# Performance work log

Measured on AMD Instinct MI355X. Metric: run time of the kernel, lower is better.

Reference implementation:

```python
import jax, jax.numpy as jnp
import numpy as np

N, E, G = 400000, 2500000, 512
IN_F, H, C = 7, 32, 2
EPS = 1e-5


def setup_inputs() -> dict:
    key = jax.random.key(0)
    ks = jax.random.split(key, 12)
    x = jax.random.normal(ks[0], (N, IN_F), jnp.float32)
    edge_index = jax.random.randint(ks[1], (2, E), 0, N, dtype=jnp.int64)
    edge_attr = jax.random.uniform(ks[2], (E,), jnp.float32)
    batch = jnp.sort(jax.random.randint(ks[3], (N,), 0, G, dtype=jnp.int64))

    def lin(k, i, o):
        return (jax.random.normal(k, (i, o), jnp.float32) / np.sqrt(i)).astype(jnp.float32)

    params = dict(
        W0=lin(ks[4], IN_F, H), b0=jnp.zeros((H,), jnp.float32),
        W1=lin(ks[5], H, H),    b1=jnp.zeros((H,), jnp.float32),
        W2=lin(ks[6], H, H),    b2=jnp.zeros((H,), jnp.float32),
        W3=lin(ks[7], H, H),    b3=jnp.zeros((H,), jnp.float32),
        bn_g=jnp.ones((3, H), jnp.float32), bn_b=jnp.zeros((3, H), jnp.float32),
        Wm0=lin(ks[8], H, H),   bm0=jnp.zeros((H,), jnp.float32),
        bnm_g=jnp.ones((H,), jnp.float32), bnm_b=jnp.zeros((H,), jnp.float32),
        Wm1=lin(ks[9], H, C),   bm1=jnp.zeros((C,), jnp.float32),
    )
    return {"x": x, "edge_index": edge_index, "edge_attr": edge_attr, "batch": batch, **params}


def _batchnorm(h, g, b):
    # training-mode batch norm over the node/graph axis
    m = h.mean(axis=0)
    v = h.var(axis=0)
    return (h - m) * jax.lax.rsqrt(v + EPS) * g + b


def _gcn_forward(x, edge_index, edge_attr, batch,
                 W0, b0, W1, b1, W2, b2, W3, b3, bn_g, bn_b,
                 Wm0, bm0, bnm_g, bnm_b, Wm1, bm1):
    row, col = edge_index[0], edge_index[1]
    # add self-loops with weight 1 (GCNConv default), then symmetric normalization
    loop = jnp.arange(N, dtype=row.dtype)
    row = jnp.concatenate([row, loop])
    col = jnp.concatenate([col, loop])
    w = jnp.concatenate([edge_attr, jnp.ones((N,), edge_attr.dtype)])
    deg = jax.ops.segment_sum(w, col, num_segments=N)
    dinv = jnp.where(deg > 0, jax.lax.rsqrt(jnp.maximum(deg, EPS)), 0.0)
    norm = dinv[row] * w * dinv[col]  # [E+N]

    def conv(h, W, b):
        h = h @ W                                    # [N,H] dense transform
        msg = norm[:, None] * h[row]                 # gather + scale
        return jax.ops.segment_sum(msg, col, num_segments=N) + b  # scatter-add

    h = jax.nn.relu(_batchnorm(conv(x, W0, b0), bn_g[0], bn_b[0]))
    h = jax.nn.relu(_batchnorm(conv(h, W1, b1), bn_g[1], bn_b[1]))
    h = jax.nn.relu(_batchnorm(conv(h, W2, b2), bn_g[2], bn_b[2]))
    h = conv(h, W3, b3)                              # last GCN layer: no norm/act

    g = jax.ops.segment_sum(h, batch, num_segments=G)  # global_add_pool -> [G,H]
    g = jax.nn.relu(_batchnorm(g @ Wm0 + bm0, bnm_g, bnm_b))
    return g @ Wm1 + bm1                             # [G,C]


def reference(x, edge_index, edge_attr, batch,
              W0, b0, W1, b1, W2, b2, W3, b3, bn_g, bn_b,
              Wm0, bm0, bnm_g, bnm_b, Wm1, bm1):
    return _gcn_forward(x, edge_index, edge_attr, batch,
                        W0, b0, W1, b1, W2, b2, W3, b3, bn_g, bn_b,
                        Wm0, bm0, bnm_g, bnm_b, Wm1, bm1)
```

## Files before the change

kernel.cpp:

```cpp
#include <hip/hip_runtime.h>

#define TPB 256
#define RBITS 10
#define RSZ   1024
#define BMAX  512
#define CHUNK 4096
constexpr float EPSV = 1e-5f;

__device__ __forceinline__ float bf2f(unsigned short u) {
  return __uint_as_float((unsigned)u << 16);
}
__device__ __forceinline__ unsigned short f2bf(float f) {
  unsigned u = __float_as_uint(f);
  return (unsigned short)((u + 0x7fffu + ((u >> 16) & 1u)) >> 16);
}


__global__ void k_bcnt(const int* __restrict__ col, int* __restrict__ bcnt, int E, int B) {
  __shared__ int h[BMAX];
  const int tid = threadIdx.x;
  for (int i = tid; i < B; i += TPB) h[i] = 0;
  __syncthreads();
  const int e0 = blockIdx.x * CHUNK;
  for (int k = tid; k < CHUNK; k += TPB) {
    int i = e0 + k;
    if (i < E) atomicAdd(&h[col[i] >> RBITS], 1);
  }
  __syncthreads();
  for (int i = tid; i < B; i += TPB)
    if (h[i]) atomicAdd(&bcnt[i], h[i]);
}

__global__ void k_bscan(const int* __restrict__ bcnt, int* __restrict__ bbase,
                        int* __restrict__ bcur, int B, int E) {
  __shared__ int red[BMAX];
  const int tid = threadIdx.x;
  int v = (tid < B) ? bcnt[tid] : 0;
  red[tid] = v;
  __syncthreads();
  for (int off = 1; off < BMAX; off <<= 1) {
    int u = (tid >= off) ? red[tid - off] : 0;
    __syncthreads();
    red[tid] += u;
    __syncthreads();
  }
  int excl = red[tid] - v;
  if (tid < B) { bbase[tid] = excl; bcur[tid] = excl; }
  if (tid == 0) bbase[B] = E;
}

__global__ void k_binfill(const int* __restrict__ row, const int* __restrict__ col,
                          const float* __restrict__ w, int* __restrict__ bcur,
                          uint2* __restrict__ buck, int E, int B) {
  __shared__ int h[BMAX], base[BMAX], cur[BMAX];
  const int tid = threadIdx.x;
  for (int i = tid; i < B; i += TPB) { h[i] = 0; cur[i] = 0; }
  __syncthreads();
  const int e0 = blockIdx.x * CHUNK;
  for (int k = tid; k < CHUNK; k += TPB) {
    int i = e0 + k;
    if (i < E) atomicAdd(&h[col[i] >> RBITS], 1);
  }
  __syncthreads();
  for (int i = tid; i < B; i += TPB)
    base[i] = h[i] ? atomicAdd(&bcur[i], h[i]) : 0;
  __syncthreads();
  for (int k = tid; k < CHUNK; k += TPB) {
    int i = e0 + k;
    if (i >= E) continue;
    int c = col[i];
    int b = c >> RBITS;
    int pos = base[b] + atomicAdd(&cur[b], 1);
    unsigned lc = (unsigned)(c & (RSZ - 1));
    buck[pos] = make_uint2((unsigned)row[i] | (lc << 19), __float_as_uint(w[i]));
  }
}

__global__ __launch_bounds__(256) void k_bucket(const uint2* __restrict__ buck,
                                                const int* __restrict__ bbase,
                                                int* __restrict__ ptr, float* __restrict__ dinv,
                                                uint2* __restrict__ pk, int N, int E) {
  __shared__ int cnt[RSZ];
  __shared__ float wsum[RSZ];
  __shared__ int lofs[RSZ];
  __shared__ int red[256];
  const int bk = blockIdx.x, tid = threadIdx.x;
  const int n0 = bk << RBITS;
  const int nloc = min(RSZ, N - n0);
  for (int i = tid; i < RSZ; i += 256) { cnt[i] = 0; wsum[i] = 0.f; }
  __syncthreads();
  const int e0 = bbase[bk], e1 = bbase[bk + 1];
  for (int i = e0 + tid; i < e1; i += 256) {
    uint2 e = buck[i];
    int lc = e.x >> 19;
    atomicAdd(&cnt[lc], 1);
    atomicAdd(&wsum[lc], __uint_as_float(e.y));
  }
  __syncthreads();
  int a = cnt[tid * 4], b = cnt[tid * 4 + 1], c = cnt[tid * 4 + 2], d = cnt[tid * 4 + 3];
  int l1 = a, l2 = a + b, l3 = a + b + c, s = a + b + c + d;
  red[tid] = s;
  __syncthreads();
  for (int off = 1; off < 256; off <<= 1) {
    int u = (tid >= off) ? red[tid - off] : 0;
    __syncthreads();
    red[tid] += u;
    __syncthreads();
  }
  int tb = red[tid] - s;
  lofs[tid * 4] = tb; lofs[tid * 4 + 1] = tb + l1;
  lofs[tid * 4 + 2] = tb + l2; lofs[tid * 4 + 3] = tb + l3;
  __syncthreads();
  for (int i = tid; i < nloc; i += 256) {
    ptr[n0 + i] = e0 + lofs[i];
    dinv[n0 + i] = rsqrtf(1.0f + wsum[i]);
  }
  for (int i = tid; i < RSZ; i += 256) cnt[i] = 0;
  __syncthreads();
  for (int i = e0 + tid; i < e1; i += 256) {
    uint2 e = buck[i];
    int lc = e.x >> 19;
    int pos = e0 + lofs[lc] + atomicAdd(&cnt[lc], 1);
    float wdc = __uint_as_float(e.y) * rsqrtf(1.0f + wsum[lc]);
    pk[pos] = make_uint2(e.x & 524287u, __float_as_uint(wdc));
  }
  if (bk == 0 && tid == 0) ptr[N] = E;
}

__global__ void k_nrme(uint2* __restrict__ pk, const float* __restrict__ dinv, int E) {
  int e = blockIdx.x * blockDim.x + threadIdx.x;
  if (e < E) {
    uint2 v = pk[e];
    pk[e].y = __float_as_uint(__uint_as_float(v.y) * dinv[v.x]);
  }
}


__global__ void k_transform0(const float* __restrict__ in, const float* __restrict__ W,
                             unsigned short* __restrict__ t, int N) {
  __shared__ float Ws[7 * 32];
  __shared__ float hs[8 * 7];
  const int tid = threadIdx.x;
  const int n0 = blockIdx.x * 8;
  if (tid < 7 * 32) Ws[tid] = W[tid];
  if (tid < 8 * 7) {
    int node = n0 + tid / 7;
    hs[tid] = (node < N) ? in[n0 * 7 + tid] : 0.0f;
  }
  __syncthreads();
  const int j = tid >> 5, c = tid & 31;
  const int node = n0 + j;
  if (node < N) {
    float acc = 0.0f;
#pragma unroll
    for (int k = 0; k < 7; ++k) acc += hs[j * 7 + k] * Ws[k * 32 + c];
    t[(size_t)node * 32 + c] = f2bf(acc);
  }
}

__global__ __launch_bounds__(256) void k_transform(
    const uint4* __restrict__ in4, const float* __restrict__ W,
    const float* __restrict__ gstats, const float* __restrict__ gamma,
    const float* __restrict__ beta, float invN, uint2* __restrict__ t2, int N) {
  __shared__ float Ws[1024];
  __shared__ float hs[32 * 33];
  __shared__ float ssb[64];
  const int tid = threadIdx.x;
  const int n0 = blockIdx.x * 32;
#pragma unroll
  for (int k = 0; k < 4; ++k) Ws[k * 256 + tid] = W[k * 256 + tid];
  if (tid < 32) {
    float m = gstats[tid] * invN;
    float v = gstats[32 + tid] * invN - m * m;
    float sc = gamma[tid] * rsqrtf(v + EPSV);
    ssb[tid] = sc;
    ssb[32 + tid] = beta[tid] - m * sc;
  }
  __syncthreads();
  if (tid < 128) {
    const int r = tid >> 2, q = tid & 3;
    const int node = n0 + r;
    uint4 v = make_uint4(0, 0, 0, 0);
    if (node < N) v = in4[(size_t)node * 4 + q];
    float* h = &hs[r * 33 + q * 8];
    const float* sc = &ssb[q * 8];
    const float* sh = &ssb[32 + q * 8];
    h[0] = fmaxf(__uint_as_float(v.x << 16) * sc[0] + sh[0], 0.f);
    h[1] = fmaxf(__uint_as_float(v.x & 0xffff0000u) * sc[1] + sh[1], 0.f);
    h[2] = fmaxf(__uint_as_float(v.y << 16) * sc[2] + sh[2], 0.f);
    h[3] = fmaxf(__uint_as_float(v.y & 0xffff0000u) * sc[3] + sh[3], 0.f);
    h[4] = fmaxf(__uint_as_float(v.z << 16) * sc[4] + sh[4], 0.f);
    h[5] = fmaxf(__uint_as_float(v.z & 0xffff0000u) * sc[5] + sh[5], 0.f);
    h[6] = fmaxf(__uint_as_float(v.w << 16) * sc[6] + sh[6], 0.f);
    h[7] = fmaxf(__uint_as_float(v.w & 0xffff0000u) * sc[7] + sh[7], 0.f);
  }
  __syncthreads();
  const int j = tid >> 3;
  const int c0 = (tid & 7) * 4;
  const int node = n0 + j;
  if (node < N) {
    float a0 = 0.f, a1 = 0.f, a2 = 0.f, a3 = 0.f;
#pragma unroll
    for (int k = 0; k < 32; ++k) {
      float v = hs[j * 33 + k];
      const float* w = &Ws[k * 32 + c0];
      a0 += v * w[0]; a1 += v * w[1]; a2 += v * w[2]; a3 += v * w[3];
    }
    uint2 o;
    o.x = (unsigned)f2bf(a0) | ((unsigned)f2bf(a1) << 16);
    o.y = (unsigned)f2bf(a2) | ((unsigned)f2bf(a3) << 16);
    t2[(size_t)node * 8 + (tid & 7)] = o;
  }
}


__device__ __forceinline__ void fma8(float* acc, uint4 v, float wt) {
  acc[0] += wt * __uint_as_float(v.x << 16);
  acc[1] += wt * __uint_as_float(v.x & 0xffff0000u);
  acc[2] += wt * __uint_as_float(v.y << 16);
  acc[3] += wt * __uint_as_float(v.y & 0xffff0000u);
  acc[4] += wt * __uint_as_float(v.z << 16);
  acc[5] += wt * __uint_as_float(v.z & 0xffff0000u);
  acc[6] += wt * __uint_as_float(v.w << 16);
  acc[7] += wt * __uint_as_float(v.w & 0xffff0000u);
}

__global__ __launch_bounds__(256, 4) void k_gather(
    const uint2* __restrict__ pk, const int* __restrict__ ptr,
    const float* __restrict__ dinv, const uint4* __restrict__ t4,
    uint4* __restrict__ out4, int N) {
  const int n = blockIdx.x * 256 + threadIdx.x;
  if (n >= N) return;
  const int p0 = ptr[n], p1 = ptr[n + 1];
  const float dvn = dinv[n];
  float acc[32];
  {
    const float wt = dvn * dvn;
    const size_t rb = (size_t)n * 4;
    uint4 A = t4[rb], B = t4[rb + 1], C = t4[rb + 2], D = t4[rb + 3];
#pragma unroll
    for (int k = 0; k < 32; ++k) acc[k] = 0.f;
    fma8(acc, A, wt); fma8(acc + 8, B, wt); fma8(acc + 16, C, wt); fma8(acc + 24, D, wt);
  }
  for (int p = p0; p < p1; ++p) {
    uint2 e = pk[p];
    const float wt = __uint_as_float(e.y);
    const size_t rb = (size_t)e.x * 4;
    uint4 A = t4[rb], B = t4[rb + 1], C = t4[rb + 2], D = t4[rb + 3];
    fma8(acc, A, wt); fma8(acc + 8, B, wt); fma8(acc + 16, C, wt); fma8(acc + 24, D, wt);
  }
  const size_t ob = (size_t)n * 4;
#pragma unroll
  for (int q = 0; q < 4; ++q) {
    uint4 o;
    o.x = (unsigned)f2bf(acc[q * 8 + 0]) | ((unsigned)f2bf(acc[q * 8 + 1]) << 16);
    o.y = (unsigned)f2bf(acc[q * 8 + 2]) | ((unsigned)f2bf(acc[q * 8 + 3]) << 16);
    o.z = (unsigned)f2bf(acc[q * 8 + 4]) | ((unsigned)f2bf(acc[q * 8 + 5]) << 16);
    o.w = (unsigned)f2bf(acc[q * 8 + 6]) | ((unsigned)f2bf(acc[q * 8 + 7]) << 16);
    out4[ob + q] = o;
  }
}


__global__ void k_stats(const uint4* __restrict__ x4, float* __restrict__ gstats, int nquads) {
  __shared__ float ls[64];
  const int tid = threadIdx.x;
  if (tid < 64) ls[tid] = 0.f;
  __syncthreads();
  const int q = tid & 3;
  float s[8], sq[8];
#pragma unroll
  for (int k = 0; k < 8; ++k) { s[k] = 0.f; sq[k] = 0.f; }
  for (int idx = blockIdx.x * TPB + tid; idx < nquads; idx += gridDim.x * TPB) {
    uint4 v = x4[idx];
    float f0 = __uint_as_float(v.x << 16), f1 = __uint_as_float(v.x & 0xffff0000u);
    float f2 = __uint_as_float(v.y << 16), f3 = __uint_as_float(v.y & 0xffff0000u);
    float f4 = __uint_as_float(v.z << 16), f5 = __uint_as_float(v.z & 0xffff0000u);
    float f6 = __uint_as_float(v.w << 16), f7 = __uint_as_float(v.w & 0xffff0000u);
    s[0] += f0; sq[0] += f0 * f0;  s[1] += f1; sq[1] += f1 * f1;
    s[2] += f2; sq[2] += f2 * f2;  s[3] += f3; sq[3] += f3 * f3;
    s[4] += f4; sq[4] += f4 * f4;  s[5] += f5; sq[5] += f5 * f5;
    s[6] += f6; sq[6] += f6 * f6;  s[7] += f7; sq[7] += f7 * f7;
  }
#pragma unroll
  for (int k = 0; k < 8; ++k) {
    int c = q * 8 + k;
    atomicAdd(&ls[c], s[k]);
    atomicAdd(&ls[32 + c], sq[k]);
  }
  __syncthreads();
  if (tid < 64) unsafeAtomicAdd(&gstats[tid], ls[tid]);
}


__global__ __launch_bounds__(256) void k_pool(
    const uint4* __restrict__ h4, const int* __restrict__ batch,
    const float* __restrict__ b3, float* __restrict__ pool, int N) {
  __shared__ float red[64 * 33];
  const int g = blockIdx.x, tid = threadIdx.x;
  int lo = 0, hi = N;
  while (lo < hi) { int mid = (lo + hi) >> 1; if (batch[mid] < g) lo = mid + 1; else hi = mid; }
  const int start = lo;
  hi = N;
  while (lo < hi) { int mid = (lo + hi) >> 1; if (batch[mid] < g + 1) lo = mid + 1; else hi = mid; }
  const int end = lo;
  const int j = tid >> 2, q = tid & 3;
  float a[8];
#pragma unroll
  for (int k = 0; k < 8; ++k) a[k] = 0.f;
  for (int i = start + j; i < end; i += 64) {
    uint4 v = h4[(size_t)i * 4 + q];
    a[0] += __uint_as_float(v.x << 16); a[1] += __uint_as_float(v.x & 0xffff0000u);
    a[2] += __uint_as_float(v.y << 16); a[3] += __uint_as_float(v.y & 0xffff0000u);
    a[4] += __uint_as_float(v.z << 16); a[5] += __uint_as_float(v.z & 0xffff0000u);
    a[6] += __uint_as_float(v.w << 16); a[7] += __uint_as_float(v.w & 0xffff0000u);
  }
#pragma unroll
  for (int k = 0; k < 8; ++k) red[j * 33 + q * 8 + k] = a[k];
  __syncthreads();
  for (int off = 32; off >= 1; off >>= 1) {
    if (j < off) {
#pragma unroll
      for (int k = 0; k < 8; ++k)
        red[j * 33 + q * 8 + k] += red[(j + off) * 33 + q * 8 + k];
    }
    __syncthreads();
  }
  if (tid < 32) pool[g * 32 + tid] = red[tid] + (float)(end - start) * b3[tid];
}


__global__ void k_mlpz(const float* __restrict__ pool, const float* __restrict__ Wm0,
                       const float* __restrict__ bm0, float* __restrict__ z,
                       float* __restrict__ mstats) {
  __shared__ float Ws[32 * 32];
  __shared__ float ps[8 * 32];
  __shared__ float ls[TPB], lq[TPB];
  const int tid = threadIdx.x;
  const int g0 = blockIdx.x * 8;
  for (int k = tid; k < 1024; k += TPB) Ws[k] = Wm0[k];
  if (tid < 256) ps[tid] = pool[g0 * 32 + tid];
  __syncthreads();
  const int j = tid >> 5, c = tid & 31;
  float acc = bm0[c];
#pragma unroll
  for (int k = 0; k < 32; ++k) acc += ps[j * 32 + k] * Ws[k * 32 + c];
  z[(g0 + j) * 32 + c] = acc;
  ls[tid] = acc;
  lq[tid] = acc * acc;
  __syncthreads();
  for (int off = 128; off >= 32; off >>= 1) {
    if (tid < off) { ls[tid] += ls[tid + off]; lq[tid] += lq[tid + off]; }
    __syncthreads();
  }
  if (tid < 32) {
    unsafeAtomicAdd(&mstats[tid], ls[tid]);
    unsafeAtomicAdd(&mstats[32 + tid], lq[tid]);
  }
}

__global__ void k_mlpfin(const float* __restrict__ z, const float* __restrict__ mstats,
                         const float* __restrict__ bng, const float* __restrict__ bnb,
                         const float* __restrict__ Wm1, const float* __restrict__ bm1,
                         float* __restrict__ out) {
  __shared__ float sc[32], sh[32], w1[64];
  const int tid = threadIdx.x;
  if (tid < 32) {
    float m = mstats[tid] * (1.0f / 512.0f);
    float v = mstats[32 + tid] * (1.0f / 512.0f) - m * m;
    float s = bng[tid] * rsqrtf(v + EPSV);
    sc[tid] = s;
    sh[tid] = bnb[tid] - m * s;
  }
  if (tid < 64) w1[tid] = Wm1[tid];
  __syncthreads();
  const int g = tid >> 1, o = tid & 1;
  float acc = bm1[o];
#pragma unroll
  for (int c = 0; c < 32; ++c) {
    float hc = fmaxf(z[g * 32 + c] * sc[c] + sh[c], 0.f);
    acc += hc * w1[c * 2 + o];
  }
  out[tid] = acc;
}


extern "C" void kernel_launch(void* const* d_in, const int* in_sizes, int n_in,
                              void* d_out, int out_size, void* d_ws, size_t ws_size,
                              hipStream_t stream) {
  const float* x     = (const float*)d_in[0];
  const int*   ei    = (const int*)d_in[1];
  const float* ea    = (const float*)d_in[2];
  const int*   batch = (const int*)d_in[3];
  const float* W0    = (const float*)d_in[4];
  const float* W1    = (const float*)d_in[6];
  const float* W2    = (const float*)d_in[8];
  const float* W3    = (const float*)d_in[10];
  const float* b3    = (const float*)d_in[11];
  const float* bng   = (const float*)d_in[12];
  const float* bnb   = (const float*)d_in[13];
  const float* Wm0   = (const float*)d_in[14];
  const float* bm0   = (const float*)d_in[15];
  const float* bnmg  = (const float*)d_in[16];
  const float* bnmb  = (const float*)d_in[17];
  const float* Wm1   = (const float*)d_in[18];
  const float* bm1   = (const float*)d_in[19];
  float* out = (float*)d_out;

  const int N = in_sizes[3];
  const int E = in_sizes[2];
  const int* row = ei;
  const int* col = ei + E;
  const int B = (N + RSZ - 1) >> RBITS;

  char* wsb = (char*)d_ws;
  auto alloc = [&](size_t bytes) { char* p = wsb; wsb += (bytes + 255) & ~size_t(255); return p; };
  int*   bcnt  = (int*)alloc((size_t)(BMAX + 1) * 4);
  int*   bbase = (int*)alloc((size_t)(BMAX + 1) * 4);
  int*   bcur  = (int*)alloc((size_t)BMAX * 4);
  int*   ptr   = (int*)alloc((size_t)(N + 1) * 4);
  uint2* buck  = (uint2*)alloc((size_t)E * 8);
  uint2* pk    = (uint2*)alloc((size_t)E * 8);
  float* dinv  = (float*)alloc((size_t)N * 4);
  unsigned short* B0 = (unsigned short*)alloc((size_t)N * 32 * 2);
  unsigned short* B1 = (unsigned short*)alloc((size_t)N * 32 * 2);
  float* stats = (float*)alloc(4 * 64 * 4);
  float* pool  = (float*)alloc(512 * 32 * 4);
  float* zbuf  = (float*)alloc(512 * 32 * 4);

  hipMemsetAsync(bcnt, 0, (size_t)(BMAX + 1) * 4, stream);
  hipMemsetAsync(stats, 0, 4 * 64 * 4, stream);

  const int nb_c = (E + CHUNK - 1) / CHUNK;
  const int nb_e = (E + 255) / 256;
  const int nb_t0 = (N + 7) / 8;
  const int nb_t = (N + 31) / 32;
  const int nb_g = (N + 255) / 256;
  const int nquads = N * 4;
  const float invN = 1.0f / (float)N;
  float* mstats = stats + 192;

  k_bcnt<<<nb_c, TPB, 0, stream>>>(col, bcnt, E, B);
  k_bscan<<<1, BMAX, 0, stream>>>(bcnt, bbase, bcur, B, E);
  k_binfill<<<nb_c, TPB, 0, stream>>>(row, col, ea, bcur, buck, E, B);
  k_bucket<<<B, 256, 0, stream>>>(buck, bbase, ptr, dinv, pk, N, E);
  k_nrme<<<nb_e, 256, 0, stream>>>(pk, dinv, E);

  k_transform0<<<nb_t0, TPB, 0, stream>>>(x, W0, B0, N);
  k_gather<<<nb_g, 256, 0, stream>>>(pk, ptr, dinv, (const uint4*)B0, (uint4*)B1, N);
  k_stats<<<1024, TPB, 0, stream>>>((const uint4*)B1, stats, nquads);

  k_transform<<<nb_t, 256, 0, stream>>>((const uint4*)B1, W1, stats, bng, bnb, invN,
                                        (uint2*)B0, N);
  k_gather<<<nb_g, 256, 0, stream>>>(pk, ptr, dinv, (const uint4*)B0, (uint4*)B1, N);
  k_stats<<<1024, TPB, 0, stream>>>((const uint4*)B1, stats + 64, nquads);

  k_transform<<<nb_t, 256, 0, stream>>>((const uint4*)B1, W2, stats + 64, bng + 32, bnb + 32,
                                        invN, (uint2*)B0, N);
  k_gather<<<nb_g, 256, 0, stream>>>(pk, ptr, dinv, (const uint4*)B0, (uint4*)B1, N);
  k_stats<<<1024, TPB, 0, stream>>>((const uint4*)B1, stats + 128, nquads);

  k_transform<<<nb_t, 256, 0, stream>>>((const uint4*)B1, W3, stats + 128, bng + 64, bnb + 64,
                                        invN, (uint2*)B0, N);
  k_gather<<<nb_g, 256, 0, stream>>>(pk, ptr, dinv, (const uint4*)B0, (uint4*)B1, N);

  k_pool<<<512, 256, 0, stream>>>((const uint4*)B1, batch, b3, pool, N);
  k_mlpz<<<64, TPB, 0, stream>>>(pool, Wm0, bm0, zbuf, mstats);
  k_mlpfin<<<1, 1024, 0, stream>>>(zbuf, mstats, bnmg, bnmb, Wm1, bm1, out);
}
```

Baseline: 740.0 us.

## Aggregate raw 7-feature input before first transform and fuse layer-0 stats

Uses linearity (A·X)·W = A·(X·W) to gather the 7-wide input packed as 8 bf16 values (16 bytes per node) instead of the 32-wide transformed features (64 bytes per node). The matmul by W0 then runs after aggregation in a new kernel that also reduces the batch-norm sums, which removes one stats pass. The gather is templated on width and now prefetches the next edge record, so pk needs one padding entry. Converting x to bf16 before aggregation changes rounding slightly, and the prefetch reads one element past the valid edge range.

```diff
diff --git a/kernel.cpp b/kernel.cpp
--- a/kernel.cpp
+++ b/kernel.cpp
@@ -136,27 +136,74 @@
 }
 
 
-__global__ void k_transform0(const float* __restrict__ in, const float* __restrict__ W,
-                             unsigned short* __restrict__ t, int N) {
+__global__ void k_packx(const float* __restrict__ x, uint4* __restrict__ g, int N) {
+  int n = blockIdx.x * 256 + threadIdx.x;
+  if (n >= N) return;
+  const float* p = x + (size_t)n * 7;
+  unsigned b[8];
+#pragma unroll
+  for (int k = 0; k < 7; ++k) b[k] = f2bf(p[k]);
+  b[7] = 0;
+  uint4 o;
+  o.x = b[0] | (b[1] << 16); o.y = b[2] | (b[3] << 16);
+  o.z = b[4] | (b[5] << 16); o.w = b[6] | (b[7] << 16);
+  g[n] = o;
+}
+
+__global__ __launch_bounds__(256) void k_transform0b(
+    const uint4* __restrict__ g1, const float* __restrict__ W,
+    float* __restrict__ gstats, uint2* __restrict__ t2, int N) {
   __shared__ float Ws[7 * 32];
-  __shared__ float hs[8 * 7];
-  const int tid = threadIdx.x;
-  const int n0 = blockIdx.x * 8;
-  if (tid < 7 * 32) Ws[tid] = W[tid];
-  if (tid < 8 * 7) {
-    int node = n0 + tid / 7;
-    hs[tid] = (node < N) ? in[n0 * 7 + tid] : 0.0f;
-  }
-  __syncthreads();
-  const int j = tid >> 5, c = tid & 31;
+  __shared__ float hs[32 * 9];
+  __shared__ float sarr[64];
+  const int tid = threadIdx.x;
+  const int n0 = blockIdx.x * 32;
+  if (tid < 224) Ws[tid] = W[tid];
+  if (tid < 64) sarr[tid] = 0.f;
+  if (tid < 32) {
+    const int node = n0 + tid;
+    uint4 v = make_uint4(0, 0, 0, 0);
+    if (node < N) v = g1[node];
+    float* h = &hs[tid * 9];
+    h[0] = __uint_as_float(v.x << 16); h[1] = __uint_as_float(v.x & 0xffff0000u);
+    h[2] = __uint_as_float(v.y << 16); h[3] = __uint_as_float(v.y & 0xffff0000u);
+    h[4] = __uint_as_float(v.z << 16); h[5] = __uint_as_float(v.z & 0xffff0000u);
+    h[6] = __uint_as_float(v.w << 16); h[7] = 0.f;
+  }
+  __syncthreads();
+  const int j = tid >> 3, q = tid & 7, c0 = q * 4;
   const int node = n0 + j;
+  float a0 = 0.f, a1 = 0.f, a2 = 0.f, a3 = 0.f;
+#pragma unroll
+  for (int k = 0; k < 7; ++k) {
+    float v = hs[j * 9 + k];
+    const float* w = &Ws[k * 32 + c0];
+    a0 += v * w[0]; a1 += v * w[1]; a2 += v * w[2]; a3 += v * w[3];
+  }
   if (node < N) {
-    float acc = 0.0f;
-#pragma unroll
-    for (int k = 0; k < 7; ++k) acc += hs[j * 7 + k] * Ws[k * 32 + c];
-    t[(size_t)node * 32 + c] = f2bf(acc);
-  }
-}
+    uint2 o;
+    o.x = (unsigned)f2bf(a0) | ((unsigned)f2bf(a1) << 16);
+    o.y = (unsigned)f2bf(a2) | ((unsigned)f2bf(a3) << 16);
+    t2[(size_t)node * 8 + q] = o;
+  }
+  float q0 = a0 * a0, q1 = a1 * a1, q2 = a2 * a2, q3 = a3 * a3;
+#pragma unroll
+  for (int m = 8; m < 64; m <<= 1) {
+    a0 += __shfl_xor(a0, m, 64); a1 += __shfl_xor(a1, m, 64);
+    a2 += __shfl_xor(a2, m, 64); a3 += __shfl_xor(a3, m, 64);
+    q0 += __shfl_xor(q0, m, 64); q1 += __shfl_xor(q1, m, 64);
+    q2 += __shfl_xor(q2, m, 64); q3 += __shfl_xor(q3, m, 64);
+  }
+  if ((tid & 63) < 8) {
+    atomicAdd(&sarr[c0 + 0], a0); atomicAdd(&sarr[c0 + 1], a1);
+    atomicAdd(&sarr[c0 + 2], a2); atomicAdd(&sarr[c0 + 3], a3);
+    atomicAdd(&sarr[32 + c0 + 0], q0); atomicAdd(&sarr[32 + c0 + 1], q1);
+    atomicAdd(&sarr[32 + c0 + 2], q2); atomicAdd(&sarr[32 + c0 + 3], q3);
+  }
+  __syncthreads();
+  if (tid < 64) unsafeAtomicAdd(&gstats[tid], sarr[tid]);
+}
+
 
 __global__ __launch_bounds__(256) void k_transform(
     const uint4* __restrict__ in4, const float* __restrict__ W,
@@ -225,6 +272,7 @@
   acc[7] += wt * __uint_as_float(v.w & 0xffff0000u);
 }
 
+template <int Q>
 __global__ __launch_bounds__(256, 4) void k_gather(
     const uint2* __restrict__ pk, const int* __restrict__ ptr,
     const float* __restrict__ dinv, const uint4* __restrict__ t4,
@@ -233,31 +281,35 @@
   if (n >= N) return;
   const int p0 = ptr[n], p1 = ptr[n + 1];
   const float dvn = dinv[n];
-  float acc[32];
+  float acc[8 * Q];
+#pragma unroll
+  for (int k = 0; k < 8 * Q; ++k) acc[k] = 0.f;
   {
     const float wt = dvn * dvn;
-    const size_t rb = (size_t)n * 4;
-    uint4 A = t4[rb], B = t4[rb + 1], C = t4[rb + 2], D = t4[rb + 3];
-#pragma unroll
-    for (int k = 0; k < 32; ++k) acc[k] = 0.f;
-    fma8(acc, A, wt); fma8(acc + 8, B, wt); fma8(acc + 16, C, wt); fma8(acc + 24, D, wt);
-  }
-  for (int p = p0; p < p1; ++p) {
-    uint2 e = pk[p];
-    const float wt = __uint_as_float(e.y);
-    const size_t rb = (size_t)e.x * 4;
-    uint4 A = t4[rb], B = t4[rb + 1], C = t4[rb + 2], D = t4[rb + 3];
-    fma8(acc, A, wt); fma8(acc + 8, B, wt); fma8(acc + 16, C, wt); fma8(acc + 24, D, wt);
-  }
-  const size_t ob = (size_t)n * 4;
-#pragma unroll
-  for (int q = 0; q < 4; ++q) {
+    const size_t rb = (size_t)n * Q;
+#pragma unroll
+    for (int qq = 0; qq < Q; ++qq) fma8(acc + 8 * qq, t4[rb + qq], wt);
+  }
+  if (p0 < p1) {
+    uint2 e = pk[p0];
+    for (int p = p0; p < p1; ++p) {
+      uint2 en = pk[p + 1];
+      const float wt = __uint_as_float(e.y);
+      const size_t rb = (size_t)e.x * Q;
+#pragma unroll
+      for (int qq = 0; qq < Q; ++qq) fma8(acc + 8 * qq, t4[rb + qq], wt);
+      e = en;
+    }
+  }
+  const size_t ob = (size_t)n * Q;
+#pragma unroll
+  for (int qq = 0; qq < Q; ++qq) {
     uint4 o;
-    o.x = (unsigned)f2bf(acc[q * 8 + 0]) | ((unsigned)f2bf(acc[q * 8 + 1]) << 16);
-    o.y = (unsigned)f2bf(acc[q * 8 + 2]) | ((unsigned)f2bf(acc[q * 8 + 3]) << 16);
-    o.z = (unsigned)f2bf(acc[q * 8 + 4]) | ((unsigned)f2bf(acc[q * 8 + 5]) << 16);
-    o.w = (unsigned)f2bf(acc[q * 8 + 6]) | ((unsigned)f2bf(acc[q * 8 + 7]) << 16);
-    out4[ob + q] = o;
+    o.x = (unsigned)f2bf(acc[qq * 8 + 0]) | ((unsigned)f2bf(acc[qq * 8 + 1]) << 16);
+    o.y = (unsigned)f2bf(acc[qq * 8 + 2]) | ((unsigned)f2bf(acc[qq * 8 + 3]) << 16);
+    o.z = (unsigned)f2bf(acc[qq * 8 + 4]) | ((unsigned)f2bf(acc[qq * 8 + 5]) << 16);
+    o.w = (unsigned)f2bf(acc[qq * 8 + 6]) | ((unsigned)f2bf(acc[qq * 8 + 7]) << 16);
+    out4[ob + qq] = o;
   }
 }
 
@@ -420,8 +472,10 @@
   int*   bcur  = (int*)alloc((size_t)BMAX * 4);
   int*   ptr   = (int*)alloc((size_t)(N + 1) * 4);
   uint2* buck  = (uint2*)alloc((size_t)E * 8);
-  uint2* pk    = (uint2*)alloc((size_t)E * 8);
+  uint2* pk    = (uint2*)alloc((size_t)(E + 1) * 8);
   float* dinv  = (float*)alloc((size_t)N * 4);
+  uint4* G0    = (uint4*)alloc((size_t)N * 16);
+  uint4* G1    = (uint4*)alloc((size_t)N * 16);
   unsigned short* B0 = (unsigned short*)alloc((size_t)N * 32 * 2);
   unsigned short* B1 = (unsigned short*)alloc((size_t)N * 32 * 2);
   float* stats = (float*)alloc(4 * 64 * 4);
@@ -433,7 +487,6 @@
 
   const int nb_c = (E + CHUNK - 1) / CHUNK;
   const int nb_e = (E + 255) / 256;
-  const int nb_t0 = (N + 7) / 8;
   const int nb_t = (N + 31) / 32;
   const int nb_g = (N + 255) / 256;
   const int nquads = N * 4;
@@ -446,23 +499,23 @@
   k_bucket<<<B, 256, 0, stream>>>(buck, bbase, ptr, dinv, pk, N, E);
   k_nrme<<<nb_e, 256, 0, stream>>>(pk, dinv, E);
 
-  k_transform0<<<nb_t0, TPB, 0, stream>>>(x, W0, B0, N);
-  k_gather<<<nb_g, 256, 0, stream>>>(pk, ptr, dinv, (const uint4*)B0, (uint4*)B1, N);
-  k_stats<<<1024, TPB, 0, stream>>>((const uint4*)B1, stats, nquads);
+  k_packx<<<nb_g, 256, 0, stream>>>(x, G0, N);
+  k_gather<1><<<nb_g, 256, 0, stream>>>(pk, ptr, dinv, G0, G1, N);
+  k_transform0b<<<nb_t, 256, 0, stream>>>(G1, W0, stats, (uint2*)B1, N);
 
   k_transform<<<nb_t, 256, 0, stream>>>((const uint4*)B1, W1, stats, bng, bnb, invN,
                                         (uint2*)B0, N);
-  k_gather<<<nb_g, 256, 0, stream>>>(pk, ptr, dinv, (const uint4*)B0, (uint4*)B1, N);
+  k_gather<4><<<nb_g, 256, 0, stream>>>(pk, ptr, dinv, (const uint4*)B0, (uint4*)B1, N);
   k_stats<<<1024, TPB, 0, stream>>>((const uint4*)B1, stats + 64, nquads);
 
   k_transform<<<nb_t, 256, 0, stream>>>((const uint4*)B1, W2, stats + 64, bng + 32, bnb + 32,
                                         invN, (uint2*)B0, N);
-  k_gather<<<nb_g, 256, 0, stream>>>(pk, ptr, dinv, (const uint4*)B0, (uint4*)B1, N);
+  k_gather<4><<<nb_g, 256, 0, stream>>>(pk, ptr, dinv, (const uint4*)B0, (uint4*)B1, N);
   k_stats<<<1024, TPB, 0, stream>>>((const uint4*)B1, stats + 128, nquads);
 
   k_transform<<<nb_t, 256, 0, stream>>>((const uint4*)B1, W3, stats + 128, bng + 64, bnb + 64,
                                         invN, (uint2*)B0, N);
-  k_gather<<<nb_g, 256, 0, stream>>>(pk, ptr, dinv, (const uint4*)B0, (uint4*)B1, N);
+  k_gather<4><<<nb_g, 256, 0, stream>>>(pk, ptr, dinv, (const uint4*)B0, (uint4*)B1, N);
 
   k_pool<<<512, 256, 0, stream>>>((const uint4*)B1, batch, b3, pool, N);
   k_mlpz<<<64, TPB, 0, stream>>>(pool, Wm0, bm0, zbuf, mstats);
```

New measurement: 984.3 us. +33.0%, slower.

## Aggregate before transform and fuse BN, ReLU and weights into the gather

Applied to the files above, without the earlier changes.

Each GCN layer now aggregates neighbor features first and applies the weight matrix in the gather epilogue, using A(hW) = (Ah)W. This removes the separate transform kernels and their full-size intermediate write and read. The previous layer's batchnorm scale/shift and ReLU are applied per gathered neighbor inside the gather. Layer 0 gathers the raw 7-wide input, packed to bf16 in 16 bytes per node by the bucket-count kernel, so its random gathers move far less data. In exchange, the gather does extra per-edge BN arithmetic and holds many more registers (accumulators plus scale/shift arrays), which may lower occupancy. The input features are also rounded to bf16 before aggregation instead of after.

```diff
diff --git a/kernel.cpp b/kernel.cpp
--- a/kernel.cpp
+++ b/kernel.cpp
@@ -16,7 +16,9 @@
 }
 
 
-__global__ void k_bcnt(const int* __restrict__ col, int* __restrict__ bcnt, int E, int B) {
+__global__ void k_bcnt(const int* __restrict__ col, int* __restrict__ bcnt,
+                       const float* __restrict__ x, uint4* __restrict__ g,
+                       int E, int B, int N) {
   __shared__ int h[BMAX];
   const int tid = threadIdx.x;
   for (int i = tid; i < B; i += TPB) h[i] = 0;
@@ -29,6 +31,17 @@
   __syncthreads();
   for (int i = tid; i < B; i += TPB)
     if (h[i]) atomicAdd(&bcnt[i], h[i]);
+  for (int n = blockIdx.x * TPB + tid; n < N; n += gridDim.x * TPB) {
+    const float* p = x + (size_t)n * 7;
+    unsigned b[8];
+#pragma unroll
+    for (int k = 0; k < 7; ++k) b[k] = f2bf(p[k]);
+    b[7] = 0;
+    uint4 o;
+    o.x = b[0] | (b[1] << 16); o.y = b[2] | (b[3] << 16);
+    o.z = b[4] | (b[5] << 16); o.w = b[6] | (b[7] << 16);
+    g[n] = o;
+  }
 }
 
 __global__ void k_bscan(const int* __restrict__ bcnt, int* __restrict__ bbase,
@@ -136,128 +149,150 @@
 }
 
 
-__global__ void k_transform0(const float* __restrict__ in, const float* __restrict__ W,
-                             unsigned short* __restrict__ t, int N) {
-  __shared__ float Ws[7 * 32];
-  __shared__ float hs[8 * 7];
-  const int tid = threadIdx.x;
-  const int n0 = blockIdx.x * 8;
-  if (tid < 7 * 32) Ws[tid] = W[tid];
-  if (tid < 8 * 7) {
-    int node = n0 + tid / 7;
-    hs[tid] = (node < N) ? in[n0 * 7 + tid] : 0.0f;
-  }
-  __syncthreads();
-  const int j = tid >> 5, c = tid & 31;
-  const int node = n0 + j;
-  if (node < N) {
-    float acc = 0.0f;
-#pragma unroll
-    for (int k = 0; k < 7; ++k) acc += hs[j * 7 + k] * Ws[k * 32 + c];
-    t[(size_t)node * 32 + c] = f2bf(acc);
-  }
-}
-
-__global__ __launch_bounds__(256) void k_transform(
-    const uint4* __restrict__ in4, const float* __restrict__ W,
-    const float* __restrict__ gstats, const float* __restrict__ gamma,
-    const float* __restrict__ beta, float invN, uint2* __restrict__ t2, int N) {
+template <int C0>
+__device__ __forceinline__ void fmaBN8(float (&acc)[32], const float (&sc)[32],
+                                       const float (&sh)[32], uint4 v, float wt) {
+  float h0 = fmaxf(__uint_as_float(v.x << 16) * sc[C0 + 0] + sh[C0 + 0], 0.f);
+  float h1 = fmaxf(__uint_as_float(v.x & 0xffff0000u) * sc[C0 + 1] + sh[C0 + 1], 0.f);
+  float h2 = fmaxf(__uint_as_float(v.y << 16) * sc[C0 + 2] + sh[C0 + 2], 0.f);
+  float h3 = fmaxf(__uint_as_float(v.y & 0xffff0000u) * sc[C0 + 3] + sh[C0 + 3], 0.f);
+  float h4 = fmaxf(__uint_as_float(v.z << 16) * sc[C0 + 4] + sh[C0 + 4], 0.f);
+  float h5 = fmaxf(__uint_as_float(v.z & 0xffff0000u) * sc[C0 + 5] + sh[C0 + 5], 0.f);
+  float h6 = fmaxf(__uint_as_float(v.w << 16) * sc[C0 + 6] + sh[C0 + 6], 0.f);
+  float h7 = fmaxf(__uint_as_float(v.w & 0xffff0000u) * sc[C0 + 7] + sh[C0 + 7], 0.f);
+  acc[C0 + 0] += wt * h0; acc[C0 + 1] += wt * h1;
+  acc[C0 + 2] += wt * h2; acc[C0 + 3] += wt * h3;
+  acc[C0 + 4] += wt * h4; acc[C0 + 5] += wt * h5;
+  acc[C0 + 6] += wt * h6; acc[C0 + 7] += wt * h7;
+}
+
+__global__ __launch_bounds__(256) void k_gatherw(
+    const uint2* __restrict__ pk, const int* __restrict__ ptr,
+    const float* __restrict__ dinv, const uint4* __restrict__ in4,
+    const float* __restrict__ W, const float* __restrict__ gstats,
+    const float* __restrict__ gamma, const float* __restrict__ beta,
+    float invN, uint4* __restrict__ out4, int N) {
   __shared__ float Ws[1024];
-  __shared__ float hs[32 * 33];
   __shared__ float ssb[64];
   const int tid = threadIdx.x;
-  const int n0 = blockIdx.x * 32;
 #pragma unroll
   for (int k = 0; k < 4; ++k) Ws[k * 256 + tid] = W[k * 256 + tid];
   if (tid < 32) {
     float m = gstats[tid] * invN;
     float v = gstats[32 + tid] * invN - m * m;
-    float sc = gamma[tid] * rsqrtf(v + EPSV);
-    ssb[tid] = sc;
-    ssb[32 + tid] = beta[tid] - m * sc;
-  }
-  __syncthreads();
-  if (tid < 128) {
-    const int r = tid >> 2, q = tid & 3;
-    const int node = n0 + r;
-    uint4 v = make_uint4(0, 0, 0, 0);
-    if (node < N) v = in4[(size_t)node * 4 + q];
-    float* h = &hs[r * 33 + q * 8];
-    const float* sc = &ssb[q * 8];
-    const float* sh = &ssb[32 + q * 8];
-    h[0] = fmaxf(__uint_as_float(v.x << 16) * sc[0] + sh[0], 0.f);
-    h[1] = fmaxf(__uint_as_float(v.x & 0xffff0000u) * sc[1] + sh[1], 0.f);
-    h[2] = fmaxf(__uint_as_float(v.y << 16) * sc[2] + sh[2], 0.f);
-    h[3] = fmaxf(__uint_as_float(v.y & 0xffff0000u) * sc[3] + sh[3], 0.f);
-    h[4] = fmaxf(__uint_as_float(v.z << 16) * sc[4] + sh[4], 0.f);
-    h[5] = fmaxf(__uint_as_float(v.z & 0xffff0000u) * sc[5] + sh[5], 0.f);
-    h[6] = fmaxf(__uint_as_float(v.w << 16) * sc[6] + sh[6], 0.f);
-    h[7] = fmaxf(__uint_as_float(v.w & 0xffff0000u) * sc[7] + sh[7], 0.f);
-  }
-  __syncthreads();
-  const int j = tid >> 3;
-  const int c0 = (tid & 7) * 4;
-  const int node = n0 + j;
-  if (node < N) {
-    float a0 = 0.f, a1 = 0.f, a2 = 0.f, a3 = 0.f;
-#pragma unroll
-    for (int k = 0; k < 32; ++k) {
-      float v = hs[j * 33 + k];
-      const float* w = &Ws[k * 32 + c0];
-      a0 += v * w[0]; a1 += v * w[1]; a2 += v * w[2]; a3 += v * w[3];
-    }
-    uint2 o;
-    o.x = (unsigned)f2bf(a0) | ((unsigned)f2bf(a1) << 16);
-    o.y = (unsigned)f2bf(a2) | ((unsigned)f2bf(a3) << 16);
-    t2[(size_t)node * 8 + (tid & 7)] = o;
-  }
-}
-
-
-__device__ __forceinline__ void fma8(float* acc, uint4 v, float wt) {
-  acc[0] += wt * __uint_as_float(v.x << 16);
-  acc[1] += wt * __uint_as_float(v.x & 0xffff0000u);
-  acc[2] += wt * __uint_as_float(v.y << 16);
-  acc[3] += wt * __uint_as_float(v.y & 0xffff0000u);
-  acc[4] += wt * __uint_as_float(v.z << 16);
-  acc[5] += wt * __uint_as_float(v.z & 0xffff0000u);
-  acc[6] += wt * __uint_as_float(v.w << 16);
-  acc[7] += wt * __uint_as_float(v.w & 0xffff0000u);
-}
-
-__global__ __launch_bounds__(256, 4) void k_gather(
-    const uint2* __restrict__ pk, const int* __restrict__ ptr,
-    const float* __restrict__ dinv, const uint4* __restrict__ t4,
-    uint4* __restrict__ out4, int N) {
-  const int n = blockIdx.x * 256 + threadIdx.x;
+    float s = gamma[tid] * rsqrtf(v + EPSV);
+    ssb[tid] = s;
+    ssb[32 + tid] = beta[tid] - m * s;
+  }
+  __syncthreads();
+  const int n = blockIdx.x * 256 + tid;
   if (n >= N) return;
+  float sc[32], sh[32];
+#pragma unroll
+  for (int c = 0; c < 32; ++c) { sc[c] = ssb[c]; sh[c] = ssb[32 + c]; }
+  float acc[32];
+#pragma unroll
+  for (int k = 0; k < 32; ++k) acc[k] = 0.f;
   const int p0 = ptr[n], p1 = ptr[n + 1];
   const float dvn = dinv[n];
-  float acc[32];
   {
     const float wt = dvn * dvn;
     const size_t rb = (size_t)n * 4;
-    uint4 A = t4[rb], B = t4[rb + 1], C = t4[rb + 2], D = t4[rb + 3];
-#pragma unroll
-    for (int k = 0; k < 32; ++k) acc[k] = 0.f;
-    fma8(acc, A, wt); fma8(acc + 8, B, wt); fma8(acc + 16, C, wt); fma8(acc + 24, D, wt);
-  }
-  for (int p = p0; p < p1; ++p) {
-    uint2 e = pk[p];
-    const float wt = __uint_as_float(e.y);
-    const size_t rb = (size_t)e.x * 4;
-    uint4 A = t4[rb], B = t4[rb + 1], C = t4[rb + 2], D = t4[rb + 3];
-    fma8(acc, A, wt); fma8(acc + 8, B, wt); fma8(acc + 16, C, wt); fma8(acc + 24, D, wt);
+    uint4 A = in4[rb], Bv = in4[rb + 1], Cv = in4[rb + 2], Dv = in4[rb + 3];
+    fmaBN8<0>(acc, sc, sh, A, wt);  fmaBN8<8>(acc, sc, sh, Bv, wt);
+    fmaBN8<16>(acc, sc, sh, Cv, wt); fmaBN8<24>(acc, sc, sh, Dv, wt);
+  }
+  if (p0 < p1) {
+    uint2 e = pk[p0];
+    for (int p = p0; p < p1; ++p) {
+      uint2 en = pk[p + 1];
+      const float wt = __uint_as_float(e.y);
+      const size_t rb = (size_t)e.x * 4;
+      uint4 A = in4[rb], Bv = in4[rb + 1], Cv = in4[rb + 2], Dv = in4[rb + 3];
+      fmaBN8<0>(acc, sc, sh, A, wt);  fmaBN8<8>(acc, sc, sh, Bv, wt);
+      fmaBN8<16>(acc, sc, sh, Cv, wt); fmaBN8<24>(acc, sc, sh, Dv, wt);
+      e = en;
+    }
   }
   const size_t ob = (size_t)n * 4;
 #pragma unroll
-  for (int q = 0; q < 4; ++q) {
-    uint4 o;
-    o.x = (unsigned)f2bf(acc[q * 8 + 0]) | ((unsigned)f2bf(acc[q * 8 + 1]) << 16);
-    o.y = (unsigned)f2bf(acc[q * 8 + 2]) | ((unsigned)f2bf(acc[q * 8 + 3]) << 16);
-    o.z = (unsigned)f2bf(acc[q * 8 + 4]) | ((unsigned)f2bf(acc[q * 8 + 5]) << 16);
-    o.w = (unsigned)f2bf(acc[q * 8 + 6]) | ((unsigned)f2bf(acc[q * 8 + 7]) << 16);
-    out4[ob + q] = o;
+  for (int g = 0; g < 4; ++g) {
+    float o[8];
+#pragma unroll
+    for (int j = 0; j < 8; ++j) {
+      float a = 0.f;
+#pragma unroll
+      for (int k = 0; k < 32; ++k) a += acc[k] * Ws[k * 32 + g * 8 + j];
+      o[j] = a;
+    }
+    uint4 ov;
+    ov.x = (unsigned)f2bf(o[0]) | ((unsigned)f2bf(o[1]) << 16);
+    ov.y = (unsigned)f2bf(o[2]) | ((unsigned)f2bf(o[3]) << 16);
+    ov.z = (unsigned)f2bf(o[4]) | ((unsigned)f2bf(o[5]) << 16);
+    ov.w = (unsigned)f2bf(o[6]) | ((unsigned)f2bf(o[7]) << 16);
+    out4[ob + g] = ov;
+  }
+}
+
+__global__ __launch_bounds__(256) void k_gatherw0(
+    const uint2* __restrict__ pk, const int* __restrict__ ptr,
+    const float* __restrict__ dinv, const uint4* __restrict__ g0,
+    const float* __restrict__ W, uint4* __restrict__ out4, int N) {
+  __shared__ float Ws[224];
+  const int tid = threadIdx.x;
+  if (tid < 224) Ws[tid] = W[tid];
+  __syncthreads();
+  const int n = blockIdx.x * 256 + tid;
+  if (n >= N) return;
+  float acc[8];
+#pragma unroll
+  for (int k = 0; k < 8; ++k) acc[k] = 0.f;
+  const int p0 = ptr[n], p1 = ptr[n + 1];
+  const float dvn = dinv[n];
+  {
+    const float wt = dvn * dvn;
+    uint4 v = g0[n];
+    acc[0] += wt * __uint_as_float(v.x << 16);
+    acc[1] += wt * __uint_as_float(v.x & 0xffff0000u);
+    acc[2] += wt * __uint_as_float(v.y << 16);
+    acc[3] += wt * __uint_as_float(v.y & 0xffff0000u);
+    acc[4] += wt * __uint_as_float(v.z << 16);
+    acc[5] += wt * __uint_as_float(v.z & 0xffff0000u);
+    acc[6] += wt * __uint_as_float(v.w << 16);
+  }
+  if (p0 < p1) {
+    uint2 e = pk[p0];
+    for (int p = p0; p < p1; ++p) {
+      uint2 en = pk[p + 1];
+      const float wt = __uint_as_float(e.y);
+      uint4 v = g0[e.x];
+      acc[0] += wt * __uint_as_float(v.x << 16);
+      acc[1] += wt * __uint_as_float(v.x & 0xffff0000u);
+      acc[2] += wt * __uint_as_float(v.y << 16);
+      acc[3] += wt * __uint_as_float(v.y & 0xffff0000u);
+      acc[4] += wt * __uint_as_float(v.z << 16);
+      acc[5] += wt * __uint_as_float(v.z & 0xffff0000u);
+      acc[6] += wt * __uint_as_float(v.w << 16);
+      e = en;
+    }
+  }
+  const size_t ob = (size_t)n * 4;
+#pragma unroll
+  for (int g = 0; g < 4; ++g) {
+    float o[8];
+#pragma unroll
+    for (int j = 0; j < 8; ++j) {
+      float a = 0.f;
+#pragma unroll
+      for (int k = 0; k < 7; ++k) a += acc[k] * Ws[k * 32 + g * 8 + j];
+      o[j] = a;
+    }
+    uint4 ov;
+    ov.x = (unsigned)f2bf(o[0]) | ((unsigned)f2bf(o[1]) << 16);
+    ov.y = (unsigned)f2bf(o[2]) | ((unsigned)f2bf(o[3]) << 16);
+    ov.z = (unsigned)f2bf(o[4]) | ((unsigned)f2bf(o[5]) << 16);
+    ov.w = (unsigned)f2bf(o[6]) | ((unsigned)f2bf(o[7]) << 16);
+    out4[ob + g] = ov;
   }
 }
 
@@ -420,10 +455,11 @@
   int*   bcur  = (int*)alloc((size_t)BMAX * 4);
   int*   ptr   = (int*)alloc((size_t)(N + 1) * 4);
   uint2* buck  = (uint2*)alloc((size_t)E * 8);
-  uint2* pk    = (uint2*)alloc((size_t)E * 8);
+  uint2* pk    = (uint2*)alloc((size_t)(E + 1) * 8);
   float* dinv  = (float*)alloc((size_t)N * 4);
-  unsigned short* B0 = (unsigned short*)alloc((size_t)N * 32 * 2);
-  unsigned short* B1 = (unsigned short*)alloc((size_t)N * 32 * 2);
+  uint4* G0    = (uint4*)alloc((size_t)N * 16);
+  unsigned short* BA = (unsigned short*)alloc((size_t)N * 32 * 2);
+  unsigned short* BB = (unsigned short*)alloc((size_t)N * 32 * 2);
   float* stats = (float*)alloc(4 * 64 * 4);
   float* pool  = (float*)alloc(512 * 32 * 4);
   float* zbuf  = (float*)alloc(512 * 32 * 4);
@@ -433,38 +469,32 @@
 
   const int nb_c = (E + CHUNK - 1) / CHUNK;
   const int nb_e = (E + 255) / 256;
-  const int nb_t0 = (N + 7) / 8;
-  const int nb_t = (N + 31) / 32;
   const int nb_g = (N + 255) / 256;
   const int nquads = N * 4;
   const float invN = 1.0f / (float)N;
   float* mstats = stats + 192;
 
-  k_bcnt<<<nb_c, TPB, 0, stream>>>(col, bcnt, E, B);
+  k_bcnt<<<nb_c, TPB, 0, stream>>>(col, bcnt, x, G0, E, B, N);
   k_bscan<<<1, BMAX, 0, stream>>>(bcnt, bbase, bcur, B, E);
   k_binfill<<<nb_c, TPB, 0, stream>>>(row, col, ea, bcur, buck, E, B);
   k_bucket<<<B, 256, 0, stream>>>(buck, bbase, ptr, dinv, pk, N, E);
   k_nrme<<<nb_e, 256, 0, stream>>>(pk, dinv, E);
 
-  k_transform0<<<nb_t0, TPB, 0, stream>>>(x, W0, B0, N);
-  k_gather<<<nb_g, 256, 0, stream>>>(pk, ptr, dinv, (const uint4*)B0, (uint4*)B1, N);
-  k_stats<<<1024, TPB, 0, stream>>>((const uint4*)B1, stats, nquads);
-
-  k_transform<<<nb_t, 256, 0, stream>>>((const uint4*)B1, W1, stats, bng, bnb, invN,
-                                        (uint2*)B0, N);
-  k_gather<<<nb_g, 256, 0, stream>>>(pk, ptr, dinv, (const uint4*)B0, (uint4*)B1, N);
-  k_stats<<<1024, TPB, 0, stream>>>((const uint4*)B1, stats + 64, nquads);
-
-  k_transform<<<nb_t, 256, 0, stream>>>((const uint4*)B1, W2, stats + 64, bng + 32, bnb + 32,
-                                        invN, (uint2*)B0, N);
-  k_gather<<<nb_g, 256, 0, stream>>>(pk, ptr, dinv, (const uint4*)B0, (uint4*)B1, N);
-  k_stats<<<1024, TPB, 0, stream>>>((const uint4*)B1, stats + 128, nquads);
-
-  k_transform<<<nb_t, 256, 0, stream>>>((const uint4*)B1, W3, stats + 128, bng + 64, bnb + 64,
-                                        invN, (uint2*)B0, N);
-  k_gather<<<nb_g, 256, 0, stream>>>(pk, ptr, dinv, (const uint4*)B0, (uint4*)B1, N);
-
-  k_pool<<<512, 256, 0, stream>>>((const uint4*)B1, batch, b3, pool, N);
+  k_gatherw0<<<nb_g, 256, 0, stream>>>(pk, ptr, dinv, G0, W0, (uint4*)BA, N);
+  k_stats<<<1024, TPB, 0, stream>>>((const uint4*)BA, stats, nquads);
+
+  k_gatherw<<<nb_g, 256, 0, stream>>>(pk, ptr, dinv, (const uint4*)BA, W1,
+                                      stats, bng, bnb, invN, (uint4*)BB, N);
+  k_stats<<<1024, TPB, 0, stream>>>((const uint4*)BB, stats + 64, nquads);
+
+  k_gatherw<<<nb_g, 256, 0, stream>>>(pk, ptr, dinv, (const uint4*)BB, W2,
+                                      stats + 64, bng + 32, bnb + 32, invN, (uint4*)BA, N);
+  k_stats<<<1024, TPB, 0, stream>>>((const uint4*)BA, stats + 128, nquads);
+
+  k_gatherw<<<nb_g, 256, 0, stream>>>(pk, ptr, dinv, (const uint4*)BA, W3,
+                                      stats + 128, bng + 64, bnb + 64, invN, (uint4*)BB, N);
+
+  k_pool<<<512, 256, 0, stream>>>((const uint4*)BB, batch, b3, pool, N);
   k_mlpz<<<64, TPB, 0, stream>>>(pool, Wm0, bm0, zbuf, mstats);
   k_mlpfin<<<1, 1024, 0, stream>>>(zbuf, mstats, bnmg, bnmb, Wm1, bm1, out);
 }
```

After: 884.8 us. 1.2x slower.
